# Kernel optimization log

Measured on AMD Instinct MI355X. Metric: run time of the kernel, lower is better.

Reference implementation:

```python
import jax, jax.numpy as jnp
import numpy as np

EMBED_DIM = 64
N_EMBED = 1024
BATCH, H, W = 16, 64, 64


def setup_inputs() -> dict:
    key = jax.random.key(0)
    k1, k2 = jax.random.split(key)
    inputs = jax.random.normal(k1, (BATCH, H, W, EMBED_DIM), dtype=jnp.float32)
    # codebook as in Quantize.build: RandomNormal(stddev=1.0), shape (embed_dim, n_embed)
    cluster_mean = jax.random.normal(k2, (EMBED_DIM, N_EMBED), dtype=jnp.float32)
    return {"inputs": inputs, "cluster_mean": cluster_mean}


def reference(inputs, cluster_mean):
    # inputs: [B,H,W,D]; cluster_mean: [D,K]
    D = cluster_mean.shape[0]
    samples = inputs.reshape(-1, D)  # [N,D]
    dist = (
        jnp.sum(samples * samples, axis=1, keepdims=True)
        - 2.0 * (samples @ cluster_mean)
        + jnp.sum(cluster_mean * cluster_mean, axis=0, keepdims=True)
    )
    cluster_index = jnp.argmin(dist, axis=1).reshape(inputs.shape[:-1])  # [B,H,W]
    quantize = cluster_mean.T[cluster_index]  # gather -> [B,H,W,D]
    q_loss = jnp.mean((quantize - jax.lax.stop_gradient(inputs)) ** 2)
    e_loss = jnp.mean((jax.lax.stop_gradient(quantize) - inputs) ** 2)
    loss = q_loss + 0.25 * e_loss
    # straight-through estimator
    outputs = inputs + jax.lax.stop_gradient(quantize - inputs)
    return outputs, cluster_index, loss
```

## Files before the change

kernel.cpp:

```cpp
#include <hip/hip_runtime.h>
#include <stdint.h>

#define NS 65536
#define D 64
#define K 1024
#define NEL 4194304
#define MARGIN 0.05f

typedef short bf16x8 __attribute__((ext_vector_type(8)));
typedef short s16x4 __attribute__((ext_vector_type(4)));
typedef float f32x4 __attribute__((ext_vector_type(4)));

static __device__ __forceinline__ unsigned short bf16_rne(float x) {
    union { float f; uint32_t u; } v; v.f = x;
    uint32_t r = v.u + 0x7FFFu + ((v.u >> 16) & 1u);
    return (unsigned short)(r >> 16);
}
static __device__ __forceinline__ float bf16f(unsigned short h) {
    union { uint32_t u; float f; } v; v.u = ((uint32_t)h) << 16;
    return v.f;
}

__global__ __launch_bounds__(256) void vq_prep(
    const float* __restrict__ cm,
    unsigned short* __restrict__ P,
    float* __restrict__ cnorm,
    double* __restrict__ acc)
{
    const int tx = threadIdx.x;
    const int col = tx & 15;
    const int dg = tx >> 4;
    const int b = blockIdx.x;
    const int k = b * 16 + col;
    if (b == 0 && tx == 0) *acc = 0.0;

    float p = 0.f;
    s16x4 hv, lv;
#pragma unroll
    for (int j = 0; j < 4; ++j) {
        float v = cm[(dg * 4 + j) * K + k];
        unsigned short hb = bf16_rne(v);
        hv[j] = (short)hb;
        lv[j] = (short)bf16_rne(v - bf16f(hb));
        p = fmaf(v, v, p);
    }
    const int lane = ((dg >> 1) & 3) * 16 + col;
    const int e0 = (dg & 1) * 4;
    unsigned short* ph = P + ((size_t)(b * 4 + (dg >> 3)) * 64 + lane) * 8 + e0;
    unsigned short* pl = P + ((size_t)(b * 4 + 2 + (dg >> 3)) * 64 + lane) * 8 + e0;
    *(s16x4*)ph = hv;
    *(s16x4*)pl = lv;

    __shared__ float pn[16][17];
    pn[col][dg] = p;
    __syncthreads();
    if (tx < 16) {
        float s = 0.f;
#pragma unroll
        for (int g = 0; g < 16; ++g) s += pn[tx][g];
        cnorm[b * 16 + tx] = s;
    }
}

__global__ __launch_bounds__(256, 4) void vq_main(
    const float* __restrict__ xin,
    const float* __restrict__ cm,
    const unsigned short* __restrict__ P,
    const float* __restrict__ cnorm,
    float* __restrict__ outq,
    float* __restrict__ outidx,
    double* __restrict__ acc_g)
{
    __shared__ char smemA[18432];
    __shared__ float cn_lds[1024];
    __shared__ int   widx[64];

    unsigned short* xh = (unsigned short*)smemA;
    unsigned short* xl = (unsigned short*)(smemA + 9216);
    float* mb1 = (float*)smemA;
    float* mb2 = (float*)(smemA + 4352);
    int*   mi1 = (int*)(smemA + 8704);
    int*   mi2 = (int*)(smemA + 13056);
    float* red = (float*)smemA;

    const int tx = threadIdx.x;
    const int S0 = blockIdx.x * 64;
    const int w = tx >> 6, l = tx & 63;
    const int quad = l >> 4, col = l & 15;

    const unsigned short* pb = P + (size_t)l * 8;

#define LDB(B0, B1, B2, B3, T) do {                                   \
        const unsigned short* q_ = pb + (size_t)(T) * 2048;           \
        B0 = *(const bf16x8*)(q_);                                    \
        B1 = *(const bf16x8*)(q_ + 512);                              \
        B2 = *(const bf16x8*)(q_ + 1024);                             \
        B3 = *(const bf16x8*)(q_ + 1536);                             \
    } while (0)

    bf16x8 c0, c1, c2, c3, n0, n1, n2, n3;
    LDB(c0, c1, c2, c3, 0);
    LDB(n0, n1, n2, n3, 1);

    {
        const int s = tx >> 2, d0 = (tx & 3) * 16;
        const float* gp = xin + (size_t)(S0 + s) * D + d0;
        bf16x8 hv0, hv1, lv0, lv1;
#pragma unroll
        for (int j = 0; j < 8; ++j) {
            float va = gp[j], vb = gp[8 + j];
            unsigned short ha = bf16_rne(va), hb = bf16_rne(vb);
            hv0[j] = (short)ha; hv1[j] = (short)hb;
            lv0[j] = (short)bf16_rne(va - bf16f(ha));
            lv1[j] = (short)bf16_rne(vb - bf16f(hb));
        }
        *(bf16x8*)(xh + s * 72 + d0)     = hv0;
        *(bf16x8*)(xh + s * 72 + d0 + 8) = hv1;
        *(bf16x8*)(xl + s * 72 + d0)     = lv0;
        *(bf16x8*)(xl + s * 72 + d0 + 8) = lv1;
#pragma unroll
        for (int q = 0; q < 4; ++q) cn_lds[q * 256 + tx] = cnorm[q * 256 + tx];
    }
    __syncthreads();

    const int srow = w * 16 + col;
    bf16x8 ahi0 = *(const bf16x8*)(xh + srow * 72 + quad * 8);
    bf16x8 ahi1 = *(const bf16x8*)(xh + srow * 72 + 32 + quad * 8);
    bf16x8 alo0 = *(const bf16x8*)(xl + srow * 72 + quad * 8);
    bf16x8 alo1 = *(const bf16x8*)(xl + srow * 72 + 32 + quad * 8);

    float b1[4], b2[4]; int i1[4], i2[4];
#pragma unroll
    for (int r = 0; r < 4; ++r) { b1[r] = -3.4e38f; b2[r] = -3.4e38f; i1[r] = 0; i2[r] = 0; }

#define COMPUTE(B0, B1, B2, B3, T) do {                                        \
        const int kc_ = (T) * 16 + col;                                        \
        const float h_ = 0.5f * cn_lds[kc_];                                   \
        f32x4 a_ = {-h_, -h_, -h_, -h_};                                       \
        a_ = __builtin_amdgcn_mfma_f32_16x16x32_bf16(ahi0, B0, a_, 0, 0, 0);   \
        a_ = __builtin_amdgcn_mfma_f32_16x16x32_bf16(ahi1, B1, a_, 0, 0, 0);   \
        a_ = __builtin_amdgcn_mfma_f32_16x16x32_bf16(ahi0, B2, a_, 0, 0, 0);   \
        a_ = __builtin_amdgcn_mfma_f32_16x16x32_bf16(ahi1, B3, a_, 0, 0, 0);   \
        a_ = __builtin_amdgcn_mfma_f32_16x16x32_bf16(alo0, B0, a_, 0, 0, 0);   \
        a_ = __builtin_amdgcn_mfma_f32_16x16x32_bf16(alo1, B1, a_, 0, 0, 0);   \
        _Pragma("unroll")                                                      \
        for (int r = 0; r < 4; ++r) {                                          \
            float v_ = a_[r];                                                  \
            bool c1_ = v_ > b1[r];                                             \
            bool c2_ = v_ > b2[r];                                             \
            b2[r] = __builtin_amdgcn_fmed3f(b1[r], v_, b2[r]);                 \
            b1[r] = fmaxf(b1[r], v_);                                          \
            i2[r] = c1_ ? i1[r] : (c2_ ? kc_ : i2[r]);                         \
            i1[r] = c1_ ? kc_ : i1[r];                                         \
        }                                                                      \
    } while (0)

    for (int t = 0; t < 64; t += 2) {
        COMPUTE(c0, c1, c2, c3, t);
        if (t + 2 < 64) LDB(c0, c1, c2, c3, t + 2);
        COMPUTE(n0, n1, n2, n3, t + 1);
        if (t + 3 < 64) LDB(n0, n1, n2, n3, t + 3);
    }

    const int sk = 4 * (tx + (tx >> 4));
#pragma unroll
    for (int r = 0; r < 4; ++r) {
        mb1[sk + r] = -2.f * b1[r];
        mb2[sk + r] = -2.f * b2[r];
        mi1[sk + r] = i1[r];
        mi2[sk + r] = i2[r];
    }
    __syncthreads();

    if (tx < 64) {
        const int mw = tx >> 4, mq = (tx >> 2) & 3, mr = tx & 3;
        float B1 = 3.4e38f, B2 = 3.4e38f; int I1 = 0, I2 = 0;
#pragma unroll
        for (int c = 0; c < 16; ++c) {
            const int tw = mw * 64 + mq * 16 + c;
            const int e = 4 * (tw + (tw >> 4)) + mr;
            float v1 = mb1[e]; int j1 = mi1[e];
            float v2 = mb2[e]; int j2 = mi2[e];
            if (v1 < B1)      { B2 = B1; I2 = I1; B1 = v1; I1 = j1; }
            else if (v1 < B2) { B2 = v1; I2 = j1; }
            if (v2 < B1)      { B2 = B1; I2 = I1; B1 = v2; I1 = j2; }
            else if (v2 < B2) { B2 = v2; I2 = j2; }
        }
        int winner = I1;
        if (B2 - B1 < MARGIN) {
            const float* xp = xin + (size_t)(S0 + tx) * D;
            float a0 = 0, a1 = 0, a2 = 0, a3 = 0, e0 = 0, e1 = 0, e2 = 0, e3 = 0;
            for (int dd = 0; dd < D; dd += 4) {
                float x0 = xp[dd], x1 = xp[dd + 1], x2 = xp[dd + 2], x3 = xp[dd + 3];
                a0 = fmaf(x0, cm[(dd + 0) * K + I1], a0);
                a1 = fmaf(x1, cm[(dd + 1) * K + I1], a1);
                a2 = fmaf(x2, cm[(dd + 2) * K + I1], a2);
                a3 = fmaf(x3, cm[(dd + 3) * K + I1], a3);
                e0 = fmaf(x0, cm[(dd + 0) * K + I2], e0);
                e1 = fmaf(x1, cm[(dd + 1) * K + I2], e1);
                e2 = fmaf(x2, cm[(dd + 2) * K + I2], e2);
                e3 = fmaf(x3, cm[(dd + 3) * K + I2], e3);
            }
            float d1 = fmaf(-2.f, (a0 + a1) + (a2 + a3), cn_lds[I1]);
            float d2 = fmaf(-2.f, (e0 + e1) + (e2 + e3), cn_lds[I2]);
            if (d2 < d1 || (d2 == d1 && I2 < I1)) winner = I2;
        }
        widx[tx] = winner;
    }
    __syncthreads();

    const int sl = tx >> 2, d0 = (tx & 3) * 16;
    const int gs = S0 + sl;
    const int wi = widx[sl];
    const int gt = wi >> 4, gc = wi & 15;
    const int qq = (d0 >> 3) & 3;
    const int gf = d0 >> 5;
    const unsigned short* gh = P + ((size_t)((gt * 4 + gf) * 64) + qq * 16 + gc) * 8;
    const unsigned short* gl = P + ((size_t)((gt * 4 + 2 + gf) * 64) + qq * 16 + gc) * 8;
    bf16x8 h0 = *(const bf16x8*)(gh);
    bf16x8 h1 = *(const bf16x8*)(gh + 128);
    bf16x8 l0 = *(const bf16x8*)(gl);
    bf16x8 l1 = *(const bf16x8*)(gl + 128);
    const float* xr = xin + (size_t)gs * D + d0;
    float* oq = outq + (size_t)gs * D + d0;
    float psum = 0.f;
#pragma unroll
    for (int g = 0; g < 4; ++g) {
        float4 xv = *(const float4*)(xr + 4 * g);
        float q0 = bf16f((unsigned short)(g < 2 ? h0[4 * g + 0] : h1[4 * g - 8 + 0])) +
                   bf16f((unsigned short)(g < 2 ? l0[4 * g + 0] : l1[4 * g - 8 + 0]));
        float q1 = bf16f((unsigned short)(g < 2 ? h0[4 * g + 1] : h1[4 * g - 8 + 1])) +
                   bf16f((unsigned short)(g < 2 ? l0[4 * g + 1] : l1[4 * g - 8 + 1]));
        float q2 = bf16f((unsigned short)(g < 2 ? h0[4 * g + 2] : h1[4 * g - 8 + 2])) +
                   bf16f((unsigned short)(g < 2 ? l0[4 * g + 2] : l1[4 * g - 8 + 2]));
        float q3 = bf16f((unsigned short)(g < 2 ? h0[4 * g + 3] : h1[4 * g - 8 + 3])) +
                   bf16f((unsigned short)(g < 2 ? l0[4 * g + 3] : l1[4 * g - 8 + 3]));
        float dx = q0 - xv.x, dy = q1 - xv.y, dz = q2 - xv.z, dw = q3 - xv.w;
        float4 o;
        o.x = xv.x + dx; o.y = xv.y + dy; o.z = xv.z + dz; o.w = xv.w + dw;
        *(float4*)(oq + 4 * g) = o;
        psum = fmaf(dx, dx, psum);
        psum = fmaf(dy, dy, psum);
        psum = fmaf(dz, dz, psum);
        psum = fmaf(dw, dw, psum);
    }

    if (tx < 64)
        outidx[S0 + tx] = (float)widx[tx];

    red[tx] = psum;
    __syncthreads();
    for (int st = 128; st > 0; st >>= 1) {
        if (tx < st) red[tx] += red[tx + st];
        __syncthreads();
    }
    if (tx == 0) atomicAdd(acc_g, (double)red[0]);
#undef LDB
#undef COMPUTE
}

__global__ void vq_finalize(const double* __restrict__ acc,
                            float* __restrict__ loss_out)
{
    float m = (float)(*acc / (double)NEL);
    *loss_out = m + 0.25f * m;
}

extern "C" void kernel_launch(void* const* d_in, const int* in_sizes, int n_in,
                              void* d_out, int out_size, void* d_ws, size_t ws_size,
                              hipStream_t stream) {
    const float* xin = (const float*)d_in[0];
    const float* cm  = (const float*)d_in[1];

    float* out     = (float*)d_out;
    float* outq    = out;
    float* outidx  = out + NEL;
    float* outloss = out + NEL + NS;

    unsigned short* P = (unsigned short*)d_ws;
    float*  cnorm = (float*)((char*)d_ws + 262144);
    double* acc   = (double*)((char*)d_ws + 266240);

    vq_prep<<<64, 256, 0, stream>>>(cm, P, cnorm, acc);
    vq_main<<<1024, 256, 0, stream>>>(xin, cm, P, cnorm, outq, outidx, acc);
    vq_finalize<<<1, 1, 0, stream>>>(acc, outloss);
}
```

Baseline: 118.0 us.

## Process 128 samples per block to reuse codebook fragments across two row groups

Each block now handles 128 samples instead of 64, so every wave computes two 16-row MFMA tiles against each codebook fragment loaded from global memory, halving codebook traffic per sample. The inputs are negated and the codebook norms pre-halved in LDS, which turns the running argmax into an argmin and drops the -2 scaling in the merge. The launch is halved to 512 blocks with launch bounds lowered to 2 blocks per unit, LDS use doubles, and the refinement margin is retuned for the new distance scale. Register pressure and lower occupancy are the trade-off.

```diff
diff --git a/kernel.cpp b/kernel.cpp
--- a/kernel.cpp
+++ b/kernel.cpp
@@ -5,7 +5,7 @@
 #define D 64
 #define K 1024
 #define NEL 4194304
-#define MARGIN 0.05f
+#define MARGIN_KEY 0.025f
 
 typedef short bf16x8 __attribute__((ext_vector_type(8)));
 typedef short s16x4 __attribute__((ext_vector_type(4)));
@@ -62,7 +62,7 @@
     }
 }
 
-__global__ __launch_bounds__(256, 4) void vq_main(
+__global__ __launch_bounds__(256, 2) void vq_main(
     const float* __restrict__ xin,
     const float* __restrict__ cm,
     const unsigned short* __restrict__ P,
@@ -71,20 +71,20 @@
     float* __restrict__ outidx,
     double* __restrict__ acc_g)
 {
-    __shared__ char smemA[18432];
+    __shared__ char smemA[36864];
     __shared__ float cn_lds[1024];
-    __shared__ int   widx[64];
+    __shared__ int   widx[128];
 
     unsigned short* xh = (unsigned short*)smemA;
-    unsigned short* xl = (unsigned short*)(smemA + 9216);
+    unsigned short* xl = (unsigned short*)(smemA + 18432);
     float* mb1 = (float*)smemA;
-    float* mb2 = (float*)(smemA + 4352);
-    int*   mi1 = (int*)(smemA + 8704);
-    int*   mi2 = (int*)(smemA + 13056);
+    float* mb2 = (float*)(smemA + 8704);
+    int*   mi1 = (int*)(smemA + 17408);
+    int*   mi2 = (int*)(smemA + 26112);
     float* red = (float*)smemA;
 
     const int tx = threadIdx.x;
-    const int S0 = blockIdx.x * 64;
+    const int S0 = blockIdx.x * 128;
     const int w = tx >> 6, l = tx & 63;
     const int quad = l >> 4, col = l & 15;
 
@@ -104,54 +104,72 @@
 
     {
         const int s = tx >> 2, d0 = (tx & 3) * 16;
-        const float* gp = xin + (size_t)(S0 + s) * D + d0;
-        bf16x8 hv0, hv1, lv0, lv1;
-#pragma unroll
-        for (int j = 0; j < 8; ++j) {
-            float va = gp[j], vb = gp[8 + j];
-            unsigned short ha = bf16_rne(va), hb = bf16_rne(vb);
-            hv0[j] = (short)ha; hv1[j] = (short)hb;
-            lv0[j] = (short)bf16_rne(va - bf16f(ha));
-            lv1[j] = (short)bf16_rne(vb - bf16f(hb));
-        }
-        *(bf16x8*)(xh + s * 72 + d0)     = hv0;
-        *(bf16x8*)(xh + s * 72 + d0 + 8) = hv1;
-        *(bf16x8*)(xl + s * 72 + d0)     = lv0;
-        *(bf16x8*)(xl + s * 72 + d0 + 8) = lv1;
-#pragma unroll
-        for (int q = 0; q < 4; ++q) cn_lds[q * 256 + tx] = cnorm[q * 256 + tx];
-    }
-    __syncthreads();
-
-    const int srow = w * 16 + col;
-    bf16x8 ahi0 = *(const bf16x8*)(xh + srow * 72 + quad * 8);
-    bf16x8 ahi1 = *(const bf16x8*)(xh + srow * 72 + 32 + quad * 8);
-    bf16x8 alo0 = *(const bf16x8*)(xl + srow * 72 + quad * 8);
-    bf16x8 alo1 = *(const bf16x8*)(xl + srow * 72 + 32 + quad * 8);
-
-    float b1[4], b2[4]; int i1[4], i2[4];
-#pragma unroll
-    for (int r = 0; r < 4; ++r) { b1[r] = -3.4e38f; b2[r] = -3.4e38f; i1[r] = 0; i2[r] = 0; }
+#pragma unroll
+        for (int half = 0; half < 2; ++half) {
+            const int ss = s + half * 64;
+            const float* gp = xin + (size_t)(S0 + ss) * D + d0;
+            bf16x8 hv0, hv1, lv0, lv1;
+#pragma unroll
+            for (int j = 0; j < 8; ++j) {
+                float va = -gp[j], vb = -gp[8 + j];
+                unsigned short ha = bf16_rne(va), hb = bf16_rne(vb);
+                hv0[j] = (short)ha; hv1[j] = (short)hb;
+                lv0[j] = (short)bf16_rne(va - bf16f(ha));
+                lv1[j] = (short)bf16_rne(vb - bf16f(hb));
+            }
+            *(bf16x8*)(xh + ss * 72 + d0)     = hv0;
+            *(bf16x8*)(xh + ss * 72 + d0 + 8) = hv1;
+            *(bf16x8*)(xl + ss * 72 + d0)     = lv0;
+            *(bf16x8*)(xl + ss * 72 + d0 + 8) = lv1;
+        }
+#pragma unroll
+        for (int q = 0; q < 4; ++q)
+            cn_lds[q * 256 + tx] = 0.5f * cnorm[q * 256 + tx];
+    }
+    __syncthreads();
+
+    bf16x8 AH0[2], AH1[2], AL0[2], AL1[2];
+#pragma unroll
+    for (int sg = 0; sg < 2; ++sg) {
+        const int srow = w * 32 + sg * 16 + col;
+        AH0[sg] = *(const bf16x8*)(xh + srow * 72 + quad * 8);
+        AH1[sg] = *(const bf16x8*)(xh + srow * 72 + 32 + quad * 8);
+        AL0[sg] = *(const bf16x8*)(xl + srow * 72 + quad * 8);
+        AL1[sg] = *(const bf16x8*)(xl + srow * 72 + 32 + quad * 8);
+    }
+
+    float b1[2][4], b2[2][4]; int i1[2][4], i2[2][4];
+#pragma unroll
+    for (int sg = 0; sg < 2; ++sg)
+#pragma unroll
+        for (int r = 0; r < 4; ++r) {
+            b1[sg][r] = 3.4e38f; b2[sg][r] = 3.4e38f;
+            i1[sg][r] = 0; i2[sg][r] = 0;
+        }
 
 #define COMPUTE(B0, B1, B2, B3, T) do {                                        \
         const int kc_ = (T) * 16 + col;                                        \
-        const float h_ = 0.5f * cn_lds[kc_];                                   \
-        f32x4 a_ = {-h_, -h_, -h_, -h_};                                       \
-        a_ = __builtin_amdgcn_mfma_f32_16x16x32_bf16(ahi0, B0, a_, 0, 0, 0);   \
-        a_ = __builtin_amdgcn_mfma_f32_16x16x32_bf16(ahi1, B1, a_, 0, 0, 0);   \
-        a_ = __builtin_amdgcn_mfma_f32_16x16x32_bf16(ahi0, B2, a_, 0, 0, 0);   \
-        a_ = __builtin_amdgcn_mfma_f32_16x16x32_bf16(ahi1, B3, a_, 0, 0, 0);   \
-        a_ = __builtin_amdgcn_mfma_f32_16x16x32_bf16(alo0, B0, a_, 0, 0, 0);   \
-        a_ = __builtin_amdgcn_mfma_f32_16x16x32_bf16(alo1, B1, a_, 0, 0, 0);   \
+        const float cv_ = cn_lds[kc_];                                         \
+        const f32x4 cc_ = {cv_, cv_, cv_, cv_};                                \
         _Pragma("unroll")                                                      \
-        for (int r = 0; r < 4; ++r) {                                          \
-            float v_ = a_[r];                                                  \
-            bool c1_ = v_ > b1[r];                                             \
-            bool c2_ = v_ > b2[r];                                             \
-            b2[r] = __builtin_amdgcn_fmed3f(b1[r], v_, b2[r]);                 \
-            b1[r] = fmaxf(b1[r], v_);                                          \
-            i2[r] = c1_ ? i1[r] : (c2_ ? kc_ : i2[r]);                         \
-            i1[r] = c1_ ? kc_ : i1[r];                                         \
+        for (int sg = 0; sg < 2; ++sg) {                                       \
+            f32x4 a_ = cc_;                                                    \
+            a_ = __builtin_amdgcn_mfma_f32_16x16x32_bf16(AH0[sg], B0, a_, 0, 0, 0); \
+            a_ = __builtin_amdgcn_mfma_f32_16x16x32_bf16(AH1[sg], B1, a_, 0, 0, 0); \
+            a_ = __builtin_amdgcn_mfma_f32_16x16x32_bf16(AH0[sg], B2, a_, 0, 0, 0); \
+            a_ = __builtin_amdgcn_mfma_f32_16x16x32_bf16(AH1[sg], B3, a_, 0, 0, 0); \
+            a_ = __builtin_amdgcn_mfma_f32_16x16x32_bf16(AL0[sg], B0, a_, 0, 0, 0); \
+            a_ = __builtin_amdgcn_mfma_f32_16x16x32_bf16(AL1[sg], B1, a_, 0, 0, 0); \
+            _Pragma("unroll")                                                  \
+            for (int r = 0; r < 4; ++r) {                                      \
+                float v_ = a_[r];                                              \
+                bool c1_ = v_ < b1[sg][r];                                     \
+                bool c2_ = v_ < b2[sg][r];                                     \
+                b2[sg][r] = __builtin_amdgcn_fmed3f(b1[sg][r], v_, b2[sg][r]); \
+                b1[sg][r] = fminf(b1[sg][r], v_);                              \
+                i2[sg][r] = c1_ ? i1[sg][r] : (c2_ ? kc_ : i2[sg][r]);         \
+                i1[sg][r] = c1_ ? kc_ : i1[sg][r];                             \
+            }                                                                  \
         }                                                                      \
     } while (0)
 
@@ -162,23 +180,28 @@
         if (t + 3 < 64) LDB(n0, n1, n2, n3, t + 3);
     }
 
-    const int sk = 4 * (tx + (tx >> 4));
-#pragma unroll
-    for (int r = 0; r < 4; ++r) {
-        mb1[sk + r] = -2.f * b1[r];
-        mb2[sk + r] = -2.f * b2[r];
-        mi1[sk + r] = i1[r];
-        mi2[sk + r] = i2[r];
-    }
-    __syncthreads();
-
-    if (tx < 64) {
-        const int mw = tx >> 4, mq = (tx >> 2) & 3, mr = tx & 3;
+    __syncthreads();
+#pragma unroll
+    for (int sg = 0; sg < 2; ++sg) {
+        const int u = (w * 2 + sg) * 64 + l;
+        const int sk = 4 * (u + (u >> 4));
+#pragma unroll
+        for (int r = 0; r < 4; ++r) {
+            mb1[sk + r] = b1[sg][r];
+            mb2[sk + r] = b2[sg][r];
+            mi1[sk + r] = i1[sg][r];
+            mi2[sk + r] = i2[sg][r];
+        }
+    }
+    __syncthreads();
+
+    if (tx < 128) {
+        const int mw = tx >> 5, msg = (tx >> 4) & 1, mq = (tx >> 2) & 3, mr = tx & 3;
         float B1 = 3.4e38f, B2 = 3.4e38f; int I1 = 0, I2 = 0;
 #pragma unroll
         for (int c = 0; c < 16; ++c) {
-            const int tw = mw * 64 + mq * 16 + c;
-            const int e = 4 * (tw + (tw >> 4)) + mr;
+            const int u = (mw * 2 + msg) * 64 + mq * 16 + c;
+            const int e = 4 * (u + (u >> 4)) + mr;
             float v1 = mb1[e]; int j1 = mi1[e];
             float v2 = mb2[e]; int j2 = mi2[e];
             if (v1 < B1)      { B2 = B1; I2 = I1; B1 = v1; I1 = j1; }
@@ -187,7 +210,7 @@
             else if (v2 < B2) { B2 = v2; I2 = j2; }
         }
         int winner = I1;
-        if (B2 - B1 < MARGIN) {
+        if (B2 - B1 < MARGIN_KEY) {
             const float* xp = xin + (size_t)(S0 + tx) * D;
             float a0 = 0, a1 = 0, a2 = 0, a3 = 0, e0 = 0, e1 = 0, e2 = 0, e3 = 0;
             for (int dd = 0; dd < D; dd += 4) {
@@ -201,53 +224,57 @@
                 e2 = fmaf(x2, cm[(dd + 2) * K + I2], e2);
                 e3 = fmaf(x3, cm[(dd + 3) * K + I2], e3);
             }
-            float d1 = fmaf(-2.f, (a0 + a1) + (a2 + a3), cn_lds[I1]);
-            float d2 = fmaf(-2.f, (e0 + e1) + (e2 + e3), cn_lds[I2]);
+            float d1 = cn_lds[I1] - ((a0 + a1) + (a2 + a3));
+            float d2 = cn_lds[I2] - ((e0 + e1) + (e2 + e3));
             if (d2 < d1 || (d2 == d1 && I2 < I1)) winner = I2;
         }
         widx[tx] = winner;
     }
     __syncthreads();
 
-    const int sl = tx >> 2, d0 = (tx & 3) * 16;
-    const int gs = S0 + sl;
-    const int wi = widx[sl];
-    const int gt = wi >> 4, gc = wi & 15;
-    const int qq = (d0 >> 3) & 3;
-    const int gf = d0 >> 5;
-    const unsigned short* gh = P + ((size_t)((gt * 4 + gf) * 64) + qq * 16 + gc) * 8;
-    const unsigned short* gl = P + ((size_t)((gt * 4 + 2 + gf) * 64) + qq * 16 + gc) * 8;
-    bf16x8 h0 = *(const bf16x8*)(gh);
-    bf16x8 h1 = *(const bf16x8*)(gh + 128);
-    bf16x8 l0 = *(const bf16x8*)(gl);
-    bf16x8 l1 = *(const bf16x8*)(gl + 128);
-    const float* xr = xin + (size_t)gs * D + d0;
-    float* oq = outq + (size_t)gs * D + d0;
     float psum = 0.f;
 #pragma unroll
-    for (int g = 0; g < 4; ++g) {
-        float4 xv = *(const float4*)(xr + 4 * g);
-        float q0 = bf16f((unsigned short)(g < 2 ? h0[4 * g + 0] : h1[4 * g - 8 + 0])) +
-                   bf16f((unsigned short)(g < 2 ? l0[4 * g + 0] : l1[4 * g - 8 + 0]));
-        float q1 = bf16f((unsigned short)(g < 2 ? h0[4 * g + 1] : h1[4 * g - 8 + 1])) +
-                   bf16f((unsigned short)(g < 2 ? l0[4 * g + 1] : l1[4 * g - 8 + 1]));
-        float q2 = bf16f((unsigned short)(g < 2 ? h0[4 * g + 2] : h1[4 * g - 8 + 2])) +
-                   bf16f((unsigned short)(g < 2 ? l0[4 * g + 2] : l1[4 * g - 8 + 2]));
-        float q3 = bf16f((unsigned short)(g < 2 ? h0[4 * g + 3] : h1[4 * g - 8 + 3])) +
-                   bf16f((unsigned short)(g < 2 ? l0[4 * g + 3] : l1[4 * g - 8 + 3]));
-        float dx = q0 - xv.x, dy = q1 - xv.y, dz = q2 - xv.z, dw = q3 - xv.w;
-        float4 o;
-        o.x = xv.x + dx; o.y = xv.y + dy; o.z = xv.z + dz; o.w = xv.w + dw;
-        *(float4*)(oq + 4 * g) = o;
-        psum = fmaf(dx, dx, psum);
-        psum = fmaf(dy, dy, psum);
-        psum = fmaf(dz, dz, psum);
-        psum = fmaf(dw, dw, psum);
-    }
-
-    if (tx < 64)
+    for (int half = 0; half < 2; ++half) {
+        const int sl = (tx >> 2) + half * 64, d0 = (tx & 3) * 16;
+        const int gs = S0 + sl;
+        const int wi = widx[sl];
+        const int gt = wi >> 4, gc = wi & 15;
+        const int qq = (d0 >> 3) & 3;
+        const int gf = d0 >> 5;
+        const unsigned short* gh = P + ((size_t)((gt * 4 + gf) * 64) + qq * 16 + gc) * 8;
+        const unsigned short* gl = P + ((size_t)((gt * 4 + 2 + gf) * 64) + qq * 16 + gc) * 8;
+        bf16x8 h0 = *(const bf16x8*)(gh);
+        bf16x8 h1 = *(const bf16x8*)(gh + 128);
+        bf16x8 l0 = *(const bf16x8*)(gl);
+        bf16x8 l1 = *(const bf16x8*)(gl + 128);
+        const float* xr = xin + (size_t)gs * D + d0;
+        float* oq = outq + (size_t)gs * D + d0;
+#pragma unroll
+        for (int g = 0; g < 4; ++g) {
+            float4 xv = *(const float4*)(xr + 4 * g);
+            float q0 = bf16f((unsigned short)(g < 2 ? h0[4 * g + 0] : h1[4 * g - 8 + 0])) +
+                       bf16f((unsigned short)(g < 2 ? l0[4 * g + 0] : l1[4 * g - 8 + 0]));
+            float q1 = bf16f((unsigned short)(g < 2 ? h0[4 * g + 1] : h1[4 * g - 8 + 1])) +
+                       bf16f((unsigned short)(g < 2 ? l0[4 * g + 1] : l1[4 * g - 8 + 1]));
+            float q2 = bf16f((unsigned short)(g < 2 ? h0[4 * g + 2] : h1[4 * g - 8 + 2])) +
+                       bf16f((unsigned short)(g < 2 ? l0[4 * g + 2] : l1[4 * g - 8 + 2]));
+            float q3 = bf16f((unsigned short)(g < 2 ? h0[4 * g + 3] : h1[4 * g - 8 + 3])) +
+                       bf16f((unsigned short)(g < 2 ? l0[4 * g + 3] : l1[4 * g - 8 + 3]));
+            float dx = q0 - xv.x, dy = q1 - xv.y, dz = q2 - xv.z, dw = q3 - xv.w;
+            float4 o;
+            o.x = xv.x + dx; o.y = xv.y + dy; o.z = xv.z + dz; o.w = xv.w + dw;
+            *(float4*)(oq + 4 * g) = o;
+            psum = fmaf(dx, dx, psum);
+            psum = fmaf(dy, dy, psum);
+            psum = fmaf(dz, dz, psum);
+            psum = fmaf(dw, dw, psum);
+        }
+    }
+
+    if (tx < 128)
         outidx[S0 + tx] = (float)widx[tx];
 
+    __syncthreads();
     red[tx] = psum;
     __syncthreads();
     for (int st = 128; st > 0; st >>= 1) {
@@ -282,6 +309,6 @@
     double* acc   = (double*)((char*)d_ws + 266240);
 
     vq_prep<<<64, 256, 0, stream>>>(cm, P, cnorm, acc);
-    vq_main<<<1024, 256, 0, stream>>>(xin, cm, P, cnorm, outq, outidx, acc);
+    vq_main<<<512, 256, 0, stream>>>(xin, cm, P, cnorm, outq, outidx, acc);
     vq_finalize<<<1, 1, 0, stream>>>(acc, outloss);
 }
```

New measurement: 125.0 us. 6.0% more time.
